# Kernel tuning notes

Measured on AMD Instinct MI355X. Metric: run time of the kernel, lower is better.

The kernel has to match this reference:

```python
import jax, jax.numpy as jnp
import numpy as np

_KX = jnp.array([[1., 0., -1.], [2., 0., -2.], [1., 0., -1.]], dtype=jnp.float32).reshape(1, 1, 3, 3)
_KY = jnp.transpose(_KX, (0, 1, 3, 2))  # ky = kx.transpose(2,3)


def _sobel(x, k):
    # x: [B,1,H,W], k: [1,1,3,3]; SAME padding=1, stride 1
    return jax.lax.conv_general_dilated(
        x, k, window_strides=(1, 1), padding=((1, 1), (1, 1)),
        dimension_numbers=('NCHW', 'OIHW', 'NCHW'))


def setup_inputs() -> dict:
    key = jax.random.key(0)
    k1, k2 = jax.random.split(key)
    sr = jax.random.normal(k1, (32, 1, 1024, 1024), dtype=jnp.float32)
    hr = jax.random.normal(k2, (32, 1, 1024, 1024), dtype=jnp.float32)
    return {"sr": sr, "hr": hr}


def reference(sr, hr):
    gx_sr = _sobel(sr, _KX)
    gy_sr = _sobel(sr, _KY)
    gx_hr = _sobel(hr, _KX)
    gy_hr = _sobel(hr, _KY)
    return jnp.mean(jnp.abs(gx_sr - gx_hr) + jnp.abs(gy_sr - gy_hr))
```

## Files before the change

### kernel.cpp

```cpp
#include <hip/hip_runtime.h>


#define IMG_H 1024
#define IMG_W 1024
#define IMG_B 32
#define WROWS 16
#define NLOAD (WROWS + 2)
#define RSTRIPS (IMG_H / WROWS)
#define NBLK (IMG_B * RSTRIPS)

struct RowBuf { float4 a, b; float ha, hb; };

__global__ __launch_bounds__(256) void edge_loss_kernel(
        const float* __restrict__ sr, const float* __restrict__ hr,
        float* __restrict__ out, float invN) {
    const int tid  = threadIdx.x;
    const int lane = tid & 63;
    const int wv   = tid >> 6;
    const int bidx = blockIdx.x;
    const int b    = bidx >> 6;
    const int ys   = bidx & 63;
    const int y0   = ys * WROWS;
    const int x0   = wv * 256 + lane * 4;
    const size_t img = (size_t)b * IMG_H * IMG_W;

    const bool edge = (lane == 0) | (lane == 63);
    const int  hx   = (lane == 0) ? x0 - 1 : x0 + 4;
    const float hm  = ((unsigned)hx < IMG_W) ? 1.f : 0.f;
    const int  hxc  = min(max(hx, 0), IMG_W - 1);

    auto LOAD = [&](int l, RowBuf& r) {
        const int rc = min(max(y0 - 1 + l, 0), IMG_H - 1);
        const size_t row = img + (size_t)rc * IMG_W;
        r.a = *reinterpret_cast<const float4*>(sr + row + x0);
        r.b = *reinterpret_cast<const float4*>(hr + row + x0);
        if (edge) { r.ha = sr[row + hxc]; r.hb = hr[row + hxc]; }
        else      { r.ha = 0.f;           r.hb = 0.f;           }
    };

    auto ST = [&](const RowBuf& r, float m, float4& s, float4& t) {
        float4 d;
        d.x = (r.a.x - r.b.x) * m;
        d.y = (r.a.y - r.b.y) * m;
        d.z = (r.a.z - r.b.z) * m;
        d.w = (r.a.w - r.b.w) * m;
        const float h = (r.ha - r.hb) * (m * hm);
        float dl = __shfl_up(d.w, 1);
        float dr = __shfl_down(d.x, 1);
        if (lane == 0)  dl = h;
        if (lane == 63) dr = h;
        s.x = dl  + 2.f * d.x + d.y;
        s.y = d.x + 2.f * d.y + d.z;
        s.z = d.y + 2.f * d.z + d.w;
        s.w = d.z + 2.f * d.w + dr;
        t.x = dl  - d.y;
        t.y = d.x - d.z;
        t.z = d.y - d.w;
        t.w = d.z - dr;
    };

    RowBuf b0, b1;
    LOAD(0, b0);
    LOAD(1, b1);

    float4 s0, t0, s1, t1, s2, t2;
    const float mT = (y0 > 0) ? 1.f : 0.f;
    ST(b0, mT, s0, t0);
    LOAD(2, b0);
    ST(b1, 1.f, s1, t1);
    LOAD(3, b1);

    float acc = 0.f;
    #pragma unroll
    for (int i = 0; i < WROWS; ++i) {
        RowBuf& cur = (i & 1) ? b1 : b0;
        const float m = ((unsigned)(y0 + i + 1) < IMG_H) ? 1.f : 0.f;
        ST(cur, m, s2, t2);
        if (i + 4 < NLOAD) LOAD(i + 4, cur);

        float gx, gy;
        gx = t0.x + 2.f * t1.x + t2.x;  gy = s0.x - s2.x;  acc += fabsf(gx) + fabsf(gy);
        gx = t0.y + 2.f * t1.y + t2.y;  gy = s0.y - s2.y;  acc += fabsf(gx) + fabsf(gy);
        gx = t0.z + 2.f * t1.z + t2.z;  gy = s0.z - s2.z;  acc += fabsf(gx) + fabsf(gy);
        gx = t0.w + 2.f * t1.w + t2.w;  gy = s0.w - s2.w;  acc += fabsf(gx) + fabsf(gy);

        s0 = s1; t0 = t1; s1 = s2; t1 = t2;
    }

    #pragma unroll
    for (int off = 32; off > 0; off >>= 1)
        acc += __shfl_down(acc, off, 64);

    __shared__ float wsum[4];
    if (lane == 0) wsum[wv] = acc;
    __syncthreads();
    if (tid == 0) {
        const float bsum = wsum[0] + wsum[1] + wsum[2] + wsum[3];
        atomicAdd(out, bsum * invN);
    }
}

extern "C" void kernel_launch(void* const* d_in, const int* in_sizes, int n_in,
                              void* d_out, int out_size, void* d_ws, size_t ws_size,
                              hipStream_t stream) {
    const float* sr = (const float*)d_in[0];
    const float* hr = (const float*)d_in[1];
    float* out = (float*)d_out;

    hipMemsetAsync(out, 0, sizeof(float), stream);

    const float invN = 1.0f / (float)((size_t)IMG_B * IMG_H * IMG_W);
    edge_loss_kernel<<<dim3(NBLK), 256, 0, stream>>>(sr, hr, out, invN);
}
```

Baseline: 280.5 us.

## Assign full image-row strip per wavefront, removing halo scalar loads

Each wavefront now processes an entire 1024-wide row strip (four float4 chunks per lane) instead of a quarter-width slice. Horizontal neighbours across chunk boundaries come from cross-lane shuffles, so the edge lanes no longer issue separate scalar halo loads and no halo is fetched twice. This raises register use per thread (double-buffered rows plus a 3-row S/T ring), and launch_bounds(256,2) caps that to keep occupancy. The block count drops fourfold, which gives more memory-level parallelism per wave but fewer waves overall.

```diff
diff --git a/kernel.cpp b/kernel.cpp
--- a/kernel.cpp
+++ b/kernel.cpp
@@ -4,87 +4,98 @@
 #define IMG_H 1024
 #define IMG_W 1024
 #define IMG_B 32
-#define WROWS 16
-#define NLOAD (WROWS + 2)
-#define RSTRIPS (IMG_H / WROWS)
-#define NBLK (IMG_B * RSTRIPS)
+#define R 16
+#define SPI (IMG_H / R)
+#define NSTRIP (IMG_B * SPI)
+#define NBLK (NSTRIP / 4)
 
-struct RowBuf { float4 a, b; float ha, hb; };
+struct Row { float4 a[4]; float4 b[4]; };
 
-__global__ __launch_bounds__(256) void edge_loss_kernel(
+__global__ __launch_bounds__(256, 2) void edge_loss_kernel(
         const float* __restrict__ sr, const float* __restrict__ hr,
         float* __restrict__ out, float invN) {
-    const int tid  = threadIdx.x;
-    const int lane = tid & 63;
-    const int wv   = tid >> 6;
-    const int bidx = blockIdx.x;
-    const int b    = bidx >> 6;
-    const int ys   = bidx & 63;
-    const int y0   = ys * WROWS;
-    const int x0   = wv * 256 + lane * 4;
+    const int tid   = threadIdx.x;
+    const int lane  = tid & 63;
+    const int wv    = tid >> 6;
+    const int strip = blockIdx.x * 4 + wv;
+    const int b     = strip >> 6;
+    const int ys    = strip & 63;
+    const int y0    = ys * R;
     const size_t img = (size_t)b * IMG_H * IMG_W;
+    const int col   = lane * 4;
 
-    const bool edge = (lane == 0) | (lane == 63);
-    const int  hx   = (lane == 0) ? x0 - 1 : x0 + 4;
-    const float hm  = ((unsigned)hx < IMG_W) ? 1.f : 0.f;
-    const int  hxc  = min(max(hx, 0), IMG_W - 1);
-
-    auto LOAD = [&](int l, RowBuf& r) {
+    auto LOAD = [&](int l, Row& r) {
         const int rc = min(max(y0 - 1 + l, 0), IMG_H - 1);
-        const size_t row = img + (size_t)rc * IMG_W;
-        r.a = *reinterpret_cast<const float4*>(sr + row + x0);
-        r.b = *reinterpret_cast<const float4*>(hr + row + x0);
-        if (edge) { r.ha = sr[row + hxc]; r.hb = hr[row + hxc]; }
-        else      { r.ha = 0.f;           r.hb = 0.f;           }
+        const float* pa = sr + img + (size_t)rc * IMG_W + col;
+        const float* pb = hr + img + (size_t)rc * IMG_W + col;
+        #pragma unroll
+        for (int q = 0; q < 4; ++q) {
+            r.a[q] = *reinterpret_cast<const float4*>(pa + q * 256);
+            r.b[q] = *reinterpret_cast<const float4*>(pb + q * 256);
+        }
     };
 
-    auto ST = [&](const RowBuf& r, float m, float4& s, float4& t) {
-        float4 d;
-        d.x = (r.a.x - r.b.x) * m;
-        d.y = (r.a.y - r.b.y) * m;
-        d.z = (r.a.z - r.b.z) * m;
-        d.w = (r.a.w - r.b.w) * m;
-        const float h = (r.ha - r.hb) * (m * hm);
-        float dl = __shfl_up(d.w, 1);
-        float dr = __shfl_down(d.x, 1);
-        if (lane == 0)  dl = h;
-        if (lane == 63) dr = h;
-        s.x = dl  + 2.f * d.x + d.y;
-        s.y = d.x + 2.f * d.y + d.z;
-        s.z = d.y + 2.f * d.z + d.w;
-        s.w = d.z + 2.f * d.w + dr;
-        t.x = dl  - d.y;
-        t.y = d.x - d.z;
-        t.z = d.y - d.w;
-        t.w = d.z - dr;
+    auto ST = [&](const Row& r, float m, float4* S, float4* T) {
+        float4 d[4];
+        #pragma unroll
+        for (int q = 0; q < 4; ++q) {
+            d[q].x = (r.a[q].x - r.b[q].x) * m;
+            d[q].y = (r.a[q].y - r.b[q].y) * m;
+            d[q].z = (r.a[q].z - r.b[q].z) * m;
+            d[q].w = (r.a[q].w - r.b[q].w) * m;
+        }
+        #pragma unroll
+        for (int q = 0; q < 4; ++q) {
+            float dl = __shfl_up(d[q].w, 1);
+            float dr = __shfl_down(d[q].x, 1);
+            const float bl = (q > 0) ? __shfl(d[q - 1].w, 63) : 0.f;
+            const float br = (q < 3) ? __shfl(d[q + 1].x, 0)  : 0.f;
+            if (lane == 0)  dl = bl;
+            if (lane == 63) dr = br;
+            S[q].x = dl     + 2.f * d[q].x + d[q].y;
+            S[q].y = d[q].x + 2.f * d[q].y + d[q].z;
+            S[q].z = d[q].y + 2.f * d[q].z + d[q].w;
+            S[q].w = d[q].z + 2.f * d[q].w + dr;
+            T[q].x = dl     - d[q].y;
+            T[q].y = d[q].x - d[q].z;
+            T[q].z = d[q].y - d[q].w;
+            T[q].w = d[q].z - dr;
+        }
     };
 
-    RowBuf b0, b1;
+    Row b0, b1;
     LOAD(0, b0);
     LOAD(1, b1);
 
-    float4 s0, t0, s1, t1, s2, t2;
+    float4 S[3][4], T[3][4];
     const float mT = (y0 > 0) ? 1.f : 0.f;
-    ST(b0, mT, s0, t0);
+    ST(b0, mT, S[0], T[0]);
     LOAD(2, b0);
-    ST(b1, 1.f, s1, t1);
+    ST(b1, 1.f, S[1], T[1]);
     LOAD(3, b1);
 
     float acc = 0.f;
     #pragma unroll
-    for (int i = 0; i < WROWS; ++i) {
-        RowBuf& cur = (i & 1) ? b1 : b0;
+    for (int i = 0; i < R; ++i) {
+        Row& cur = (i & 1) ? b1 : b0;
+        const int l = i + 2;
         const float m = ((unsigned)(y0 + i + 1) < IMG_H) ? 1.f : 0.f;
-        ST(cur, m, s2, t2);
-        if (i + 4 < NLOAD) LOAD(i + 4, cur);
+        ST(cur, m, S[(i + 2) % 3], T[(i + 2) % 3]);
+        if (l + 2 <= R + 1) LOAD(l + 2, cur);
 
-        float gx, gy;
-        gx = t0.x + 2.f * t1.x + t2.x;  gy = s0.x - s2.x;  acc += fabsf(gx) + fabsf(gy);
-        gx = t0.y + 2.f * t1.y + t2.y;  gy = s0.y - s2.y;  acc += fabsf(gx) + fabsf(gy);
-        gx = t0.z + 2.f * t1.z + t2.z;  gy = s0.z - s2.z;  acc += fabsf(gx) + fabsf(gy);
-        gx = t0.w + 2.f * t1.w + t2.w;  gy = s0.w - s2.w;  acc += fabsf(gx) + fabsf(gy);
-
-        s0 = s1; t0 = t1; s1 = s2; t1 = t2;
+        #pragma unroll
+        for (int q = 0; q < 4; ++q) {
+            const float4 t0 = T[i % 3][q];
+            const float4 t1 = T[(i + 1) % 3][q];
+            const float4 t2 = T[(i + 2) % 3][q];
+            const float4 s0 = S[i % 3][q];
+            const float4 s2 = S[(i + 2) % 3][q];
+            float gx, gy;
+            gx = t0.x + 2.f * t1.x + t2.x;  gy = s0.x - s2.x;  acc += fabsf(gx) + fabsf(gy);
+            gx = t0.y + 2.f * t1.y + t2.y;  gy = s0.y - s2.y;  acc += fabsf(gx) + fabsf(gy);
+            gx = t0.z + 2.f * t1.z + t2.z;  gy = s0.z - s2.z;  acc += fabsf(gx) + fabsf(gy);
+            gx = t0.w + 2.f * t1.w + t2.w;  gy = s0.w - s2.w;  acc += fabsf(gx) + fabsf(gy);
+        }
     }
 
     #pragma unroll
```

After: 281.8 us. Within noise of the previous version (+0.5%).
